# Performance work log

Hardware: AMD Instinct MI355X
Metric: run time of the kernel (lower is better)

The kernel has to match this reference:

```python
import jax, jax.numpy as jnp
import numpy as np

CUTOFF = 0.5


def setup_inputs() -> dict:
    key = jax.random.key(0)
    k_z, k_d, k_w, k_mu, k_sg = jax.random.split(key, 5)
    N, D_IN, D_OUT = 8192, 128, 128
    z = jax.random.normal(k_z, (N, D_IN), dtype=jnp.float32)
    dist_matrix = jax.random.uniform(k_d, (N, N), dtype=jnp.float32)
    W = jax.random.normal(k_w, (D_IN, D_OUT), dtype=jnp.float32)
    B = jnp.zeros((D_OUT,), dtype=jnp.float32)
    mu = jax.random.normal(k_mu, (1,), dtype=jnp.float32)
    sigma = jax.random.normal(k_sg, (1,), dtype=jnp.float32)
    return {"z": z, "dist_matrix": dist_matrix, "W": W, "B": B, "mu": mu, "sigma": sigma}


def reference(z, dist_matrix, W, B, mu, sigma):
    N = dist_matrix.shape[0]
    # transform every source node once: h[j] = z[j] @ W + B   [N, D_OUT]
    h = z @ W + B
    # pair mask: within cutoff and i != j
    mask = (dist_matrix < CUTOFF) & (~jnp.eye(N, dtype=bool))
    # safe distance to avoid inf/nan where masked out (original skips those pairs)
    r = jnp.where(mask, dist_matrix, 1.0)
    sens = jnp.exp(-(1.0 / r - 1.0 / mu[0]) ** 2 / (2.0 * sigma[0] ** 2))
    S = jnp.where(mask, sens, 0.0)  # [N, N]
    # z_inter[i] = sum_j S[i, j] * h[j]
    return S @ h
```

## Files before the change

kernel.cpp:

```cpp
#include <hip/hip_runtime.h>
#include <hip/hip_bf16.h>

#define NN 8192
#define DD 128
#define BM 16
#define JS 8
#define RPB 128
#define JSLICE 1024
#define KBLK 128
#define LSTR 272

typedef __attribute__((ext_vector_type(4))) float f32x4;
typedef __attribute__((ext_vector_type(8))) short bf16x8;

__device__ __forceinline__ unsigned short f2bf(float x) {
    unsigned u = __float_as_uint(x);
    u += 0x7fffu + ((u >> 16) & 1u);
    return (unsigned short)(u >> 16);
}

__global__ void __launch_bounds__(256) h_transform(
    const float* __restrict__ z, const float* __restrict__ W,
    const float* __restrict__ Bv, unsigned short* __restrict__ hT) {
    __shared__ float zs[BM * DD];
    __shared__ float wt[DD * 132];
    const int t = threadIdx.x;
    const int j0 = blockIdx.x * BM;

    {
        const f32x4* zsrc = (const f32x4*)(z + (size_t)j0 * DD);
        f32x4* zdst = (f32x4*)zs;
        zdst[t] = zsrc[t];
        zdst[t + 256] = zsrc[t + 256];
    }
    for (int q = t; q < DD * 32; q += 256) {
        int k = q >> 5;
        int n0 = (q & 31) << 2;
        f32x4 wv = *(const f32x4*)(W + k * DD + n0);
        wt[(n0 + 0) * 132 + k] = wv[0];
        wt[(n0 + 1) * 132 + k] = wv[1];
        wt[(n0 + 2) * 132 + k] = wv[2];
        wt[(n0 + 3) * 132 + k] = wv[3];
    }
    __syncthreads();

    const int n = t >> 1;
    const int ja = (t & 1) << 3;
    float acc[8];
    float bn = Bv[n];
#pragma unroll
    for (int e = 0; e < 8; e++) acc[e] = bn;

#pragma unroll 8
    for (int k4 = 0; k4 < 32; ++k4) {
        f32x4 wv = *(const f32x4*)&wt[n * 132 + (k4 << 2)];
#pragma unroll
        for (int e = 0; e < 8; e++) {
            f32x4 zv = *(const f32x4*)&zs[(ja + e) * DD + (k4 << 2)];
            acc[e] += zv[0] * wv[0] + zv[1] * wv[1] + zv[2] * wv[2] + zv[3] * wv[3];
        }
    }

    const int j = j0 + ja;
    unsigned short* dst = hT + (size_t)n * NN + j;
    uint4 uv;
    uv.x = (unsigned)f2bf(acc[0]) | ((unsigned)f2bf(acc[1]) << 16);
    uv.y = (unsigned)f2bf(acc[2]) | ((unsigned)f2bf(acc[3]) << 16);
    uv.z = (unsigned)f2bf(acc[4]) | ((unsigned)f2bf(acc[5]) << 16);
    uv.w = (unsigned)f2bf(acc[6]) | ((unsigned)f2bf(acc[7]) << 16);
    *(uint4*)dst = uv;
}

__global__ void __launch_bounds__(512, 4) fused_interact(
    const float* __restrict__ dist, const unsigned short* __restrict__ hT,
    const float* __restrict__ mu, const float* __restrict__ sigma,
    float* __restrict__ part) {
    __shared__ char s_lds[RPB * LSTR];
    __shared__ char h_lds[DD * LSTR];

    const int t = threadIdx.x;
    const int w = t >> 6;
    const int l = t & 63;
    const int rb = (int)blockIdx.x >> 3;
    const int js = (int)blockIdx.x & 7;
    const int r0 = rb * RPB;

    const int dr = t >> 5;
    const int dc = (t & 31) << 2;
    const int hn = t >> 4;
    const int hc = (t & 15) << 3;

    const int fr = l & 15;
    const int fq = l >> 4;
    const int a_base = (w * 16 + fr) * LSTR + fq * 16;
    const int b_base = fr * LSTR + fq * 16;

    const float inv_mu = 1.0f / mu[0];
    const float sg = sigma[0];
    const float ninv2s2 = -1.0f / (2.0f * sg * sg);

    f32x4 acc[8];
#pragma unroll
    for (int f = 0; f < 8; ++f) acc[f] = (f32x4){0.f, 0.f, 0.f, 0.f};

#pragma unroll 1
    for (int chunk = 0; chunk < JSLICE / KBLK; ++chunk) {
        const int jc = js * JSLICE + chunk * KBLK;

        f32x4 dv[8];
        uint4 hv[4];
#pragma unroll
        for (int p = 0; p < 8; ++p)
            dv[p] = *(const f32x4*)(dist + (size_t)(r0 + p * 16 + dr) * NN +
                                    jc + dc);
#pragma unroll
        for (int q = 0; q < 4; ++q)
            hv[q] = *(const uint4*)(hT + (size_t)(hn + q * 32) * NN + jc + hc);

        __syncthreads();

#pragma unroll
        for (int q = 0; q < 4; ++q)
            *(uint4*)(h_lds + (hn + q * 32) * LSTR + (hc << 1)) = hv[q];

#pragma unroll
        for (int p = 0; p < 8; ++p) {
            const int rloc = p * 16 + dr;
            const int rg = r0 + rloc;
            unsigned short h[4];
#pragma unroll
            for (int e = 0; e < 4; ++e) {
                float d = dv[p][e];
                float q = __builtin_amdgcn_rcpf(d) - inv_mu;
                float s = __expf(q * q * ninv2s2);
                bool keep = (d < 0.5f) & ((jc + dc + e) != rg);
                h[e] = f2bf(keep ? s : 0.0f);
            }
            uint2 u;
            u.x = (unsigned)h[0] | ((unsigned)h[1] << 16);
            u.y = (unsigned)h[2] | ((unsigned)h[3] << 16);
            *(uint2*)(s_lds + rloc * LSTR + (dc << 1)) = u;
        }

        __syncthreads();

#pragma unroll
        for (int ks = 0; ks < 4; ++ks) {
            bf16x8 a = *(const bf16x8*)(s_lds + a_base + ks * 64);
#pragma unroll
            for (int f = 0; f < 8; ++f) {
                bf16x8 b =
                    *(const bf16x8*)(h_lds + b_base + f * (16 * LSTR) + ks * 64);
                acc[f] = __builtin_amdgcn_mfma_f32_16x16x32_bf16(a, b, acc[f],
                                                                 0, 0, 0);
            }
        }
    }

    float* po = part + (size_t)js * (NN * DD);
    const int orow = r0 + w * 16 + (fq << 2);
#pragma unroll
    for (int f = 0; f < 8; ++f)
#pragma unroll
        for (int rr = 0; rr < 4; ++rr)
            po[(size_t)(orow + rr) * DD + f * 16 + fr] = acc[f][rr];
}

__global__ void __launch_bounds__(256) reduce_part(
    const float* __restrict__ part, float* __restrict__ outp) {
    const size_t idx = ((size_t)blockIdx.x * 256 + threadIdx.x) << 2;
    f32x4 s = *(const f32x4*)(part + idx);
#pragma unroll
    for (int ksp = 1; ksp < JS; ++ksp)
        s += *(const f32x4*)(part + (size_t)ksp * (NN * DD) + idx);
    *(f32x4*)(outp + idx) = s;
}

extern "C" void kernel_launch(void* const* d_in, const int* in_sizes, int n_in,
                              void* d_out, int out_size, void* d_ws, size_t ws_size,
                              hipStream_t stream) {
    const float* z = (const float*)d_in[0];
    const float* dist = (const float*)d_in[1];
    const float* W = (const float*)d_in[2];
    const float* Bv = (const float*)d_in[3];
    const float* mu = (const float*)d_in[4];
    const float* sigma = (const float*)d_in[5];
    float* out = (float*)d_out;

    unsigned short* hT = (unsigned short*)d_ws;
    const size_t hT_bytes = (size_t)DD * NN * 2;
    float* part = (float*)((char*)d_ws + hT_bytes);

    h_transform<<<NN / BM, 256, 0, stream>>>(z, W, Bv, hT);
    fused_interact<<<(NN / RPB) * JS, 512, 0, stream>>>(dist, hT, mu, sigma,
                                                        part);
    reduce_part<<<(NN * DD) / 1024, 256, 0, stream>>>(part, out);
}
```

Before: 127.9 us.

## Use single-wave blocks with fragment-ordered h layout loaded directly into registers

The h transform now writes h in a pre-swizzled fragment layout so each MFMA B operand can be loaded straight from global memory into registers, with a three-slot register ring for prefetch. The interaction kernel moves to one wave per block handling 16 rows, with only the sensitivity tile staged through a small LDS buffer, and block-level barriers are removed. This avoids the LDS round trip and syncs for h, but each 16-row block reloads all of its h slice from global or L2, so traffic to that level rises sharply and the large register arrays may limit occupancy.

Measured after the change: 127.3 us. No clear change (-0.5%).

```diff
diff --git a/kernel.cpp b/kernel.cpp
--- a/kernel.cpp
+++ b/kernel.cpp
@@ -5,13 +5,10 @@
 #define DD 128
 #define BM 16
 #define JS 8
-#define RPB 128
-#define JSLICE 1024
-#define KBLK 128
-#define LSTR 272
 
 typedef __attribute__((ext_vector_type(4))) float f32x4;
 typedef __attribute__((ext_vector_type(8))) short bf16x8;
+typedef __attribute__((ext_vector_type(4))) unsigned int u32x4;
 
 __device__ __forceinline__ unsigned short f2bf(float x) {
     unsigned u = __float_as_uint(x);
@@ -62,7 +59,8 @@
     }
 
     const int j = j0 + ja;
-    unsigned short* dst = hT + (size_t)n * NN + j;
+    unsigned short* dst = hT + ((j >> 5) * 4096 + (n >> 4) * 512 +
+                                (((j >> 3) & 3) << 7) + ((n & 15) << 3));
     uint4 uv;
     uv.x = (unsigned)f2bf(acc[0]) | ((unsigned)f2bf(acc[1]) << 16);
     uv.y = (unsigned)f2bf(acc[2]) | ((unsigned)f2bf(acc[3]) << 16);
@@ -71,99 +69,96 @@
     *(uint4*)dst = uv;
 }
 
-__global__ void __launch_bounds__(512, 4) fused_interact(
+__global__ void __launch_bounds__(64, 2) fused_interact(
     const float* __restrict__ dist, const unsigned short* __restrict__ hT,
     const float* __restrict__ mu, const float* __restrict__ sigma,
     float* __restrict__ part) {
-    __shared__ char s_lds[RPB * LSTR];
-    __shared__ char h_lds[DD * LSTR];
-
-    const int t = threadIdx.x;
-    const int w = t >> 6;
-    const int l = t & 63;
-    const int rb = (int)blockIdx.x >> 3;
-    const int js = (int)blockIdx.x & 7;
-    const int r0 = rb * RPB;
-
-    const int dr = t >> 5;
-    const int dc = (t & 31) << 2;
-    const int hn = t >> 4;
-    const int hc = (t & 15) << 3;
-
-    const int fr = l & 15;
-    const int fq = l >> 4;
-    const int a_base = (w * 16 + fr) * LSTR + fq * 16;
-    const int b_base = fr * LSTR + fq * 16;
+    __shared__ char sfr[8 * 1056];
+    const int l = threadIdx.x;
+    const int ks = (int)blockIdx.x & 7;
+    const int rt = (int)blockIdx.x >> 3;
+    const int kbeg = ks * (NN / JS);
+    const int r0 = rt * 16;
 
     const float inv_mu = 1.0f / mu[0];
     const float sg = sigma[0];
     const float ninv2s2 = -1.0f / (2.0f * sg * sg);
 
+    const float* dbase = dist + (size_t)r0 * NN + kbeg + 4 * l;
+    const unsigned short* hp = hT + (size_t)(kbeg >> 5) * 4096 + l * 8;
+
+    const int ard = (4 * (l & 15) + (l >> 4)) * 16;
+    const int awr = (l >> 3) * 1056 + ((l & 7) >> 1) * 16 + (l & 1) * 8;
+    const int colb = kbeg + 4 * l;
+
     f32x4 acc[8];
 #pragma unroll
     for (int f = 0; f < 8; ++f) acc[f] = (f32x4){0.f, 0.f, 0.f, 0.f};
 
-#pragma unroll 1
-    for (int chunk = 0; chunk < JSLICE / KBLK; ++chunk) {
-        const int jc = js * JSLICE + chunk * KBLK;
+    f32x4 dv[16];
+    u32x4 hS[3][8];
 
-        f32x4 dv[8];
-        uint4 hv[4];
-#pragma unroll
-        for (int p = 0; p < 8; ++p)
-            dv[p] = *(const f32x4*)(dist + (size_t)(r0 + p * 16 + dr) * NN +
-                                    jc + dc);
-#pragma unroll
-        for (int q = 0; q < 4; ++q)
-            hv[q] = *(const uint4*)(hT + (size_t)(hn + q * 32) * NN + jc + hc);
+#define LDDIST(SC)                                                           \
+    do {                                                                     \
+        _Pragma("unroll") for (int p = 0; p < 16; ++p)                       \
+            dv[p] = *(const f32x4*)(dbase + (size_t)p * NN + (SC) * 256);    \
+    } while (0)
 
-        __syncthreads();
+#define LDHT(SLOT, KT)                                                       \
+    do {                                                                     \
+        _Pragma("unroll") for (int f = 0; f < 8; ++f)                        \
+            hS[SLOT][f] = *(const u32x4*)(hp + (KT) * 4096 + f * 512);       \
+    } while (0)
+
+    LDDIST(0);
+    LDHT(0, 0);
+    LDHT(1, 1);
+    LDHT(2, 2);
 
 #pragma unroll
-        for (int q = 0; q < 4; ++q)
-            *(uint4*)(h_lds + (hn + q * 32) * LSTR + (hc << 1)) = hv[q];
-
+    for (int sc = 0; sc < 4; ++sc) {
 #pragma unroll
-        for (int p = 0; p < 8; ++p) {
-            const int rloc = p * 16 + dr;
-            const int rg = r0 + rloc;
-            unsigned short h[4];
+        for (int p = 0; p < 16; ++p) {
+            const int rg = r0 + p;
+            unsigned short hh[4];
 #pragma unroll
             for (int e = 0; e < 4; ++e) {
                 float d = dv[p][e];
-                float q = __builtin_amdgcn_rcpf(d) - inv_mu;
-                float s = __expf(q * q * ninv2s2);
-                bool keep = (d < 0.5f) & ((jc + dc + e) != rg);
-                h[e] = f2bf(keep ? s : 0.0f);
+                float qq = __builtin_amdgcn_rcpf(d) - inv_mu;
+                float s = __expf(qq * qq * ninv2s2);
+                bool keep = (d < 0.5f) & ((colb + sc * 256 + e) != rg);
+                hh[e] = f2bf(keep ? s : 0.0f);
             }
             uint2 u;
-            u.x = (unsigned)h[0] | ((unsigned)h[1] << 16);
-            u.y = (unsigned)h[2] | ((unsigned)h[3] << 16);
-            *(uint2*)(s_lds + rloc * LSTR + (dc << 1)) = u;
+            u.x = (unsigned)hh[0] | ((unsigned)hh[1] << 16);
+            u.y = (unsigned)hh[2] | ((unsigned)hh[3] << 16);
+            *(uint2*)(sfr + awr + p * 64) = u;
         }
-
-        __syncthreads();
+        if (sc < 3) LDDIST(sc + 1);
 
 #pragma unroll
-        for (int ks = 0; ks < 4; ++ks) {
-            bf16x8 a = *(const bf16x8*)(s_lds + a_base + ks * 64);
+        for (int g = 0; g < 8; ++g) {
+            const int kt = sc * 8 + g;
+            bf16x8 a = *(const bf16x8*)(sfr + g * 1056 + ard);
 #pragma unroll
-            for (int f = 0; f < 8; ++f) {
-                bf16x8 b =
-                    *(const bf16x8*)(h_lds + b_base + f * (16 * LSTR) + ks * 64);
-                acc[f] = __builtin_amdgcn_mfma_f32_16x16x32_bf16(a, b, acc[f],
-                                                                 0, 0, 0);
-            }
+            for (int f = 0; f < 8; ++f)
+                acc[f] = __builtin_amdgcn_mfma_f32_16x16x32_bf16(
+                    a, __builtin_bit_cast(bf16x8, hS[kt % 3][f]), acc[f],
+                    0, 0, 0);
+            if (kt + 3 < 32) LDHT((kt + 3) % 3, kt + 3);
         }
     }
+#undef LDDIST
+#undef LDHT
 
-    float* po = part + (size_t)js * (NN * DD);
-    const int orow = r0 + w * 16 + (fq << 2);
+    float* po = part + (size_t)ks * (NN * DD);
+    const int orow = r0 + ((l >> 4) << 2);
+    const int ocol = l & 15;
 #pragma unroll
     for (int f = 0; f < 8; ++f)
 #pragma unroll
         for (int rr = 0; rr < 4; ++rr)
-            po[(size_t)(orow + rr) * DD + f * 16 + fr] = acc[f][rr];
+            po[(size_t)(orow + rr) * DD + f * 16 + ocol] = acc[f][rr];
 }
 
 __global__ void __launch_bounds__(256) reduce_part(
@@ -192,7 +187,7 @@
     float* part = (float*)((char*)d_ws + hT_bytes);
 
     h_transform<<<NN / BM, 256, 0, stream>>>(z, W, Bv, hT);
-    fused_interact<<<(NN / RPB) * JS, 512, 0, stream>>>(dist, hT, mu, sigma,
-                                                        part);
+    fused_interact<<<(NN / 16) * JS, 64, 0, stream>>>(dist, hT, mu, sigma,
+                                                      part);
     reduce_part<<<(NN * DD) / 1024, 256, 0, stream>>>(part, out);
 }
```

## Build S fragments in registers directly from dist, skipping LDS staging

Applied to the files above, without the earlier changes.

Each lane now loads its own dist values in MFMA A-operand layout, computes the sensitivity weights and packs them straight into bf16x8 registers, so the S tile no longer goes through shared memory. The h tile chunk grows to 256 columns with a wider LDS stride, and dist loads are double-buffered in registers across a manually pipelined inner loop. This removes LDS writes, reads and one barrier per chunk for S. The cost is per-lane strided 32-byte global reads of dist, which coalesce less well, and higher register pressure.

New measurement: 147.4 us. +15.2%, slower.

```diff
diff --git a/kernel.cpp b/kernel.cpp
--- a/kernel.cpp
+++ b/kernel.cpp
@@ -7,8 +7,8 @@
 #define JS 8
 #define RPB 128
 #define JSLICE 1024
-#define KBLK 128
-#define LSTR 272
+#define JCHUNK 256
+#define LSTR 528
 
 typedef __attribute__((ext_vector_type(4))) float f32x4;
 typedef __attribute__((ext_vector_type(8))) short bf16x8;
@@ -75,8 +75,7 @@
     const float* __restrict__ dist, const unsigned short* __restrict__ hT,
     const float* __restrict__ mu, const float* __restrict__ sigma,
     float* __restrict__ part) {
-    __shared__ char s_lds[RPB * LSTR];
-    __shared__ char h_lds[DD * LSTR];
+    __shared__ char hs[DD * LSTR];
 
     const int t = threadIdx.x;
     const int w = t >> 6;
@@ -84,86 +83,109 @@
     const int rb = (int)blockIdx.x >> 3;
     const int js = (int)blockIdx.x & 7;
     const int r0 = rb * RPB;
-
-    const int dr = t >> 5;
-    const int dc = (t & 31) << 2;
-    const int hn = t >> 4;
-    const int hc = (t & 15) << 3;
-
-    const int fr = l & 15;
-    const int fq = l >> 4;
-    const int a_base = (w * 16 + fr) * LSTR + fq * 16;
-    const int b_base = fr * LSTR + fq * 16;
+    const int rbase = r0 + w * 16;
+
+    const int row = l & 15;
+    const int kc8 = (l >> 4) << 3;
+    const int q16 = (l >> 4) << 4;
 
     const float inv_mu = 1.0f / mu[0];
     const float sg = sigma[0];
     const float ninv2s2 = -1.0f / (2.0f * sg * sg);
 
+    const float* dp0 = dist + (size_t)(rbase + row) * NN + kc8;
+    const int diag0 = rbase + row;
+    const char* hbase = hs + row * LSTR + q16;
+
     f32x4 acc[8];
 #pragma unroll
     for (int f = 0; f < 8; ++f) acc[f] = (f32x4){0.f, 0.f, 0.f, 0.f};
 
+    f32x4 dAa, dAb, dBa, dBb;
+
+#define LOADD(Da, Db, K)                                                     \
+    do {                                                                     \
+        Da = *(const f32x4*)(dp0 + (K));                                     \
+        Db = *(const f32x4*)(dp0 + (K) + 4);                                 \
+    } while (0)
+
+#define COMPUTE(Da, Db, K, LK)                                               \
+    do {                                                                     \
+        float v0[4] = {Da[0], Da[1], Da[2], Da[3]};                          \
+        float v1[4] = {Db[0], Db[1], Db[2], Db[3]};                          \
+        unsigned short hh[8];                                                \
+        _Pragma("unroll") for (int e = 0; e < 4; ++e) {                      \
+            float d = v0[e];                                                 \
+            float qq = __builtin_amdgcn_rcpf(d) - inv_mu;                    \
+            float s = __expf(qq * qq * ninv2s2);                             \
+            bool keep = (d < 0.5f) & (((K) + kc8 + e) != diag0);             \
+            hh[e] = f2bf(keep ? s : 0.0f);                                   \
+        }                                                                    \
+        _Pragma("unroll") for (int e = 0; e < 4; ++e) {                      \
+            float d = v1[e];                                                 \
+            float qq = __builtin_amdgcn_rcpf(d) - inv_mu;                    \
+            float s = __expf(qq * qq * ninv2s2);                             \
+            bool keep = (d < 0.5f) & (((K) + kc8 + 4 + e) != diag0);         \
+            hh[4 + e] = f2bf(keep ? s : 0.0f);                               \
+        }                                                                    \
+        uint4 au;                                                            \
+        au.x = (unsigned)hh[0] | ((unsigned)hh[1] << 16);                    \
+        au.y = (unsigned)hh[2] | ((unsigned)hh[3] << 16);                    \
+        au.z = (unsigned)hh[4] | ((unsigned)hh[5] << 16);                    \
+        au.w = (unsigned)hh[6] | ((unsigned)hh[7] << 16);                    \
+        bf16x8 a0 = __builtin_bit_cast(bf16x8, au);                          \
+        _Pragma("unroll") for (int f = 0; f < 8; ++f) {                      \
+            bf16x8 bb = *(const bf16x8*)(hbase + f * (16 * LSTR) + (LK));    \
+            acc[f] = __builtin_amdgcn_mfma_f32_16x16x32_bf16(a0, bb, acc[f], \
+                                                             0, 0, 0);       \
+        }                                                                    \
+    } while (0)
+
 #pragma unroll 1
-    for (int chunk = 0; chunk < JSLICE / KBLK; ++chunk) {
-        const int jc = js * JSLICE + chunk * KBLK;
-
-        f32x4 dv[8];
-        uint4 hv[4];
-#pragma unroll
-        for (int p = 0; p < 8; ++p)
-            dv[p] = *(const f32x4*)(dist + (size_t)(r0 + p * 16 + dr) * NN +
-                                    jc + dc);
-#pragma unroll
-        for (int q = 0; q < 4; ++q)
-            hv[q] = *(const uint4*)(hT + (size_t)(hn + q * 32) * NN + jc + hc);
-
+    for (int chunk = 0; chunk < JSLICE / JCHUNK; ++chunk) {
+        const int jc = js * JSLICE + chunk * JCHUNK;
+
+        uint4 tmp[8];
+#pragma unroll
+        for (int i = 0; i < 8; ++i) {
+            int c = i * 512 + t;
+            int n = c >> 5;
+            int cb = c & 31;
+            tmp[i] = *(const uint4*)(hT + (size_t)n * NN + jc + cb * 8);
+        }
         __syncthreads();
-
-#pragma unroll
-        for (int q = 0; q < 4; ++q)
-            *(uint4*)(h_lds + (hn + q * 32) * LSTR + (hc << 1)) = hv[q];
-
-#pragma unroll
-        for (int p = 0; p < 8; ++p) {
-            const int rloc = p * 16 + dr;
-            const int rg = r0 + rloc;
-            unsigned short h[4];
-#pragma unroll
-            for (int e = 0; e < 4; ++e) {
-                float d = dv[p][e];
-                float q = __builtin_amdgcn_rcpf(d) - inv_mu;
-                float s = __expf(q * q * ninv2s2);
-                bool keep = (d < 0.5f) & ((jc + dc + e) != rg);
-                h[e] = f2bf(keep ? s : 0.0f);
-            }
-            uint2 u;
-            u.x = (unsigned)h[0] | ((unsigned)h[1] << 16);
-            u.y = (unsigned)h[2] | ((unsigned)h[3] << 16);
-            *(uint2*)(s_lds + rloc * LSTR + (dc << 1)) = u;
-        }
-
+#pragma unroll
+        for (int i = 0; i < 8; ++i) {
+            int c = i * 512 + t;
+            int n = c >> 5;
+            int cb = c & 31;
+            *(uint4*)(hs + n * LSTR + cb * 16) = tmp[i];
+        }
         __syncthreads();
 
-#pragma unroll
-        for (int ks = 0; ks < 4; ++ks) {
-            bf16x8 a = *(const bf16x8*)(s_lds + a_base + ks * 64);
-#pragma unroll
-            for (int f = 0; f < 8; ++f) {
-                bf16x8 b =
-                    *(const bf16x8*)(h_lds + b_base + f * (16 * LSTR) + ks * 64);
-                acc[f] = __builtin_amdgcn_mfma_f32_16x16x32_bf16(a, b, acc[f],
-                                                                 0, 0, 0);
-            }
-        }
-    }
+        LOADD(dAa, dAb, jc);
+        LOADD(dBa, dBb, jc + 32);
+#pragma unroll 1
+        for (int it = 0; it < 8; it += 2) {
+            const int kg = jc + (it << 5);
+            const int lk = it << 6;
+            COMPUTE(dAa, dAb, kg, lk);
+            if (it + 2 < 8) LOADD(dAa, dAb, kg + 64);
+            COMPUTE(dBa, dBb, kg + 32, lk + 64);
+            if (it + 3 < 8) LOADD(dBa, dBb, kg + 96);
+        }
+    }
+#undef LOADD
+#undef COMPUTE
 
     float* po = part + (size_t)js * (NN * DD);
-    const int orow = r0 + w * 16 + (fq << 2);
+    const int orow = rbase + ((l >> 4) << 2);
+    const int ocol = l & 15;
 #pragma unroll
     for (int f = 0; f < 8; ++f)
 #pragma unroll
         for (int rr = 0; rr < 4; ++rr)
-            po[(size_t)(orow + rr) * DD + f * 16 + fr] = acc[f][rr];
+            po[(size_t)(orow + rr) * DD + f * 16 + ocol] = acc[f][rr];
 }
 
 __global__ void __launch_bounds__(256) reduce_part(
```
